# Kernel optimization log

Measured on AMD Instinct MI355X. Metric: run time of the kernel, lower is better.

Reference implementation:

```python
import jax, jax.numpy as jnp
import numpy as np
import math

N = 4264          # all_node_num
B = 256           # batch size
VIS = 784 + 50    # input_node_num + label_node_num
NG = 8            # number of color groups (Pegasus chromatic number is small)
GS = N // NG      # 533 nodes per group
SAMPLE_NUM = 10   # Gibbs sweeps (default 1000 in source; reduced for reference)
AVG_DEG = 15.0    # Pegasus graph degree ~15


def setup_inputs() -> dict:
    key = jax.random.key(0)
    k1, k2, k3, k4 = jax.random.split(key, 4)
    # spin state in {-1, +1}, shape [B, N]
    m = jnp.where(jax.random.normal(k1, (B, N)) >= 0, 1.0, -1.0).astype(jnp.float32)
    # sparse symmetric coupling matrix J: ~AVG_DEG neighbors per node, values randn*0.01
    upper_mask = jnp.triu(jax.random.uniform(k2, (N, N)) < (AVG_DEG / N), k=1)
    Jup = jax.random.normal(k3, (N, N), dtype=jnp.float32) * 0.01 * upper_mask
    J = Jup + Jup.T
    # bias H: log-odds constant on visible nodes, zero on hidden
    h_vis = math.log((VIS / N) / (1.0 - VIS / N))
    H = jnp.zeros((N,), dtype=jnp.float32).at[:VIS].set(h_vis)
    # color groups: disjoint partition of node indices, [NG, GS]
    groups = jax.random.permutation(k4, N).reshape(NG, GS).astype(jnp.int32)
    return {"m": m, "J": J, "H": H, "groups": groups, "sample_num": SAMPLE_NUM}


def reference(m, J, H, groups, sample_num):
    n_groups = groups.shape[0]

    def sweep(m, key):
        keys = jax.random.split(key, n_groups)
        for g in range(n_groups):          # small fixed set of color groups
            idx = groups[g]                # [GS]
            # I = sparse.mm(J[idx], m.T).T + H[idx]  ->  [B, GS]
            I = jnp.einsum('bn,gn->bg', m, J[idx]) + H[idx]
            r = jax.random.uniform(keys[g], I.shape, dtype=I.dtype) * 2.0 - 1.0
            m = m.at[:, idx].set(jnp.sign(jnp.tanh(I) - r))
        return m, None

    iter_keys = jax.random.split(jax.random.key(42), sample_num)
    m, _ = jax.lax.scan(sweep, m, iter_keys)
    return m
```

## Files before the change

### kernel.cpp

```cpp
#include <hip/hip_runtime.h>
#include <hip/hip_bf16.h>
#include <stdint.h>

#define NN 4264
#define BB 256
#define GSZ 533
#define NGRP 8
#define NSWEEP 10
#define NSTEP (NSWEEP * NGRP)
#define DMAX 48
#define DFIX 24
#define NF4 1066
#define NIT 17

struct Keys { unsigned k0[NSTEP]; unsigned k1[NSTEP]; };

#define TF_ROUND(x0, x1, r) { x0 += x1; x1 = (x1 << (r)) | (x1 >> (32 - (r))); x1 ^= x0; }
#define TF_BODY(K0, K1, C0, C1, O0, O1) {                                   \
  unsigned ks0 = (K0), ks1 = (K1), ks2 = (K0) ^ (K1) ^ 0x1BD11BDAu;          \
  unsigned x0 = (C0) + ks0, x1 = (C1) + ks1;                                 \
  TF_ROUND(x0, x1, 13) TF_ROUND(x0, x1, 15) TF_ROUND(x0, x1, 26) TF_ROUND(x0, x1, 6)  \
  x0 += ks1; x1 += ks2 + 1u;                                                 \
  TF_ROUND(x0, x1, 17) TF_ROUND(x0, x1, 29) TF_ROUND(x0, x1, 16) TF_ROUND(x0, x1, 24) \
  x0 += ks2; x1 += ks0 + 2u;                                                 \
  TF_ROUND(x0, x1, 13) TF_ROUND(x0, x1, 15) TF_ROUND(x0, x1, 26) TF_ROUND(x0, x1, 6)  \
  x0 += ks0; x1 += ks1 + 3u;                                                 \
  TF_ROUND(x0, x1, 17) TF_ROUND(x0, x1, 29) TF_ROUND(x0, x1, 16) TF_ROUND(x0, x1, 24) \
  x0 += ks1; x1 += ks2 + 4u;                                                 \
  TF_ROUND(x0, x1, 13) TF_ROUND(x0, x1, 15) TF_ROUND(x0, x1, 26) TF_ROUND(x0, x1, 6)  \
  x0 += ks2; x1 += ks0 + 5u;                                                 \
  (O0) = x0; (O1) = x1; }

static void tf_host(unsigned k0, unsigned k1, unsigned c0, unsigned c1,
                    unsigned* o0, unsigned* o1) {
  unsigned a, b;
  TF_BODY(k0, k1, c0, c1, a, b);
  *o0 = a; *o1 = b;
}

__device__ __forceinline__ void tf_dev(unsigned k0, unsigned k1, unsigned c0, unsigned c1,
                                       unsigned& o0, unsigned& o1) {
  TF_BODY(k0, k1, c0, c1, o0, o1);
}

__global__ __launch_bounds__(256) void build_ell(const float* __restrict__ J,
                                                 const int* __restrict__ groups,
                                                 unsigned* __restrict__ pack4,
                                                 int2* __restrict__ exact8,
                                                 int* __restrict__ deg,
                                                 float* __restrict__ marg) {
  const int wv = threadIdx.x >> 6, lane = threadIdx.x & 63;
  const int p = blockIdx.x * 4 + wv;
  if (p >= NN) return;
  const int node = groups[p];
  const float4* row = (const float4*)(J + (size_t)node * NN);

  float4 vv[NIT];
#pragma unroll
  for (int it = 0; it < NIT; ++it) {
    const int q = it * 64 + lane;
    vv[it] = (q < NF4) ? row[q] : make_float4(0.0f, 0.0f, 0.0f, 0.0f);
  }

  int cnt = 0;
  float asum = 0.0f;
#pragma unroll
  for (int it = 0; it < NIT; ++it) {
    const float4 v = vv[it];
    const int c0 = (it * 64 + lane) * 4;
#define COMP(X, CIDX) {                                                        \
      const bool nz = ((X) != 0.0f);                                           \
      const unsigned long long mk = __ballot(nz);                              \
      const int rk = cnt + __popcll(mk & ((1ull << lane) - 1ull));             \
      if (nz) {                                                                \
        if (rk < DFIX) {                                                       \
          const unsigned bits = __float_as_uint(X);                            \
          const unsigned bf = (bits + 0x7fffu + ((bits >> 16) & 1u)) >> 16;    \
          pack4[(size_t)p * DFIX + rk] = (bf << 16) | ((unsigned)(CIDX) << 2); \
          asum += fabsf(X);                                                    \
        }                                                                      \
        if (rk < DMAX)                                                         \
          exact8[(size_t)p * DMAX + rk] = make_int2((CIDX), __float_as_int(X));\
      }                                                                        \
      cnt += __popcll(mk); }
    COMP(v.x, c0 + 0) COMP(v.y, c0 + 1) COMP(v.z, c0 + 2) COMP(v.w, c0 + 3)
#undef COMP
  }
  for (int k = cnt + lane; k < DFIX; k += 64) pack4[(size_t)p * DFIX + k] = 0u;
  for (int s = 1; s < 64; s <<= 1) asum += __shfl_xor(asum, s, 64);
  if (lane == 0) {
    deg[p] = (cnt > DMAX) ? DMAX : cnt;
    marg[p] = asum * 0.001953125f + 2e-5f;
  }
}

__global__ __launch_bounds__(576) void gibbs(const float* __restrict__ m0,
                                             const float* __restrict__ H,
                                             const int* __restrict__ groups,
                                             const unsigned* __restrict__ pack4,
                                             const int2* __restrict__ exact8,
                                             const int* __restrict__ deg,
                                             const float* __restrict__ marg,
                                             float* __restrict__ out,
                                             Keys keys) {
  __shared__ float m_lds[NN];
  const int b = blockIdx.x;
  const int i = threadIdx.x;
  const bool active = (i < GSZ);

  for (int n = i; n < NN; n += 576) m_lds[n] = m0[(size_t)b * NN + n];

  int nodeg[NGRP];
  float hg[NGRP], mgg[NGRP];
  int dgg[NGRP];
  if (active) {
#pragma unroll
    for (int g = 0; g < NGRP; ++g) {
      const int p = g * GSZ + i;
      nodeg[g] = groups[p];
      hg[g] = H[nodeg[g]];
      dgg[g] = deg[p];
      mgg[g] = marg[p];
    }
  }

  const unsigned c = (unsigned)(b * GSZ + i);

  uint4 w0, w1, w2, w3, w4, w5;
  if (active) {
    const uint4* q = (const uint4*)(pack4 + (size_t)(0 * GSZ + i) * DFIX);
    w0 = q[0]; w1 = q[1]; w2 = q[2]; w3 = q[3]; w4 = q[4]; w5 = q[5];
  }
  __syncthreads();

#pragma unroll 1
  for (int t = 0; t < NSWEEP; ++t) {
#pragma unroll
    for (int g = 0; g < NGRP; ++g) {
      const int step = t * NGRP + g;
      const unsigned k0 = keys.k0[step];
      const unsigned k1 = keys.k1[step];
      float nv = 0.0f;
      uint4 n0, n1, n2, n3, n4, n5;
      if (active) {
        unsigned o0, o1;
        tf_dev(k0, k1, 0u, c, o0, o1);
        const unsigned bits = o0 ^ o1;
        const float u = __uint_as_float((bits >> 9) | 0x3f800000u) - 1.0f;
        const float r = u * 2.0f - 1.0f;

        float a0 = 0.0f, a1 = 0.0f, a2 = 0.0f, a3 = 0.0f;
#define MV(W)  (*(const float*)((const char*)m_lds + ((W) & 0xFFFCu)))
#define ACC(W) \
        a0 += __uint_as_float((W).x & 0xFFFF0000u) * MV((W).x); \
        a1 += __uint_as_float((W).y & 0xFFFF0000u) * MV((W).y); \
        a2 += __uint_as_float((W).z & 0xFFFF0000u) * MV((W).z); \
        a3 += __uint_as_float((W).w & 0xFFFF0000u) * MV((W).w);
        ACC(w0) ACC(w1) ACC(w2) ACC(w3) ACC(w4) ACC(w5)
#undef ACC
#undef MV

        {
          const int gn = (g + 1) & (NGRP - 1);
          const uint4* qn = (const uint4*)(pack4 + (size_t)(gn * GSZ + i) * DFIX);
          n0 = qn[0]; n1 = qn[1]; n2 = qn[2]; n3 = qn[3]; n4 = qn[4]; n5 = qn[5];
        }

        const int dg = dgg[g];
        const int2* ep = exact8 + (size_t)(g * GSZ + i) * DMAX;
        if (__builtin_expect(dg > DFIX, 0)) {
          for (int k = DFIX; k < dg; ++k) {
            const int2 e = ep[k];
            a0 += __int_as_float(e.y) * m_lds[e.x];
          }
        }
        const float I = ((a0 + a1) + (a2 + a3)) + hg[g];

        const float th = tanhf(I);
        const float d = th - r;
        if (__builtin_expect(fabsf(d) > mgg[g], 1)) {
          nv = (d > 0.0f) ? 1.0f : -1.0f;
        } else {
          double I64 = (double)hg[g];
          for (int k = 0; k < dg; ++k) {
            const int2 e = ep[k];
            I64 += (double)__int_as_float(e.y) * (double)m_lds[e.x];
          }
          const double diff = tanh(I64) - (double)r;
          nv = (diff > 0.0) ? 1.0f : ((diff < 0.0) ? -1.0f : 0.0f);
        }
      }
      __syncthreads();
      if (active) m_lds[nodeg[g]] = nv;
      __syncthreads();
      w0 = n0; w1 = n1; w2 = n2; w3 = n3; w4 = n4; w5 = n5;
    }
  }

  for (int n = i; n < NN; n += 576) out[(size_t)b * NN + n] = m_lds[n];
}

extern "C" void kernel_launch(void* const* d_in, const int* in_sizes, int n_in,
                              void* d_out, int out_size, void* d_ws, size_t ws_size,
                              hipStream_t stream) {
  const float* m0     = (const float*)d_in[0];
  const float* J      = (const float*)d_in[1];
  const float* H      = (const float*)d_in[2];
  const int*   groups = (const int*)d_in[3];

  char* ws = (char*)d_ws;
  unsigned* pack4  = (unsigned*)ws;                     ws += (size_t)NN * DFIX * 4;
  int2*     exact8 = (int2*)ws;                         ws += (size_t)NN * DMAX * 8;
  int*      deg    = (int*)ws;                          ws += (size_t)NN * 4;
  float*    marg   = (float*)ws;

  Keys keys;
  for (int t = 0; t < NSWEEP; ++t) {
    unsigned ik0, ik1;
    tf_host(0u, 42u, 0u, (unsigned)t, &ik0, &ik1);
    for (int g = 0; g < NGRP; ++g) {
      unsigned gk0, gk1;
      tf_host(ik0, ik1, 0u, (unsigned)g, &gk0, &gk1);
      keys.k0[t * NGRP + g] = gk0;
      keys.k1[t * NGRP + g] = gk1;
    }
  }

  build_ell<<<(NN + 3) / 4, 256, 0, stream>>>(J, groups, pack4, exact8, deg, marg);
  gibbs<<<BB, 576, 0, stream>>>(m0, H, groups, pack4, exact8, deg, marg,
                                (float*)d_out, keys);
}
```

Baseline: 298.3 us.

## Precompute atanh of random thresholds in a separate kernel, compare in pre-activation space

Adds a kernel that generates every Threefry uniform for all steps and stores atanh(r) in a large workspace table. The Gibbs kernel then compares I against atanh(r), which removes tanhf and the per-step Threefry hash from the sequential loop. It prefetches the next step's value and drops the register double-buffering of the ELL packs, reloading them each step instead. In exchange it pays for an extra launch and for writing and reading about 44 MB of table. It needs enough workspace, otherwise it falls back to the old path.

```diff
diff --git a/kernel.cpp b/kernel.cpp
--- a/kernel.cpp
+++ b/kernel.cpp
@@ -8,6 +8,7 @@
 #define NGRP 8
 #define NSWEEP 10
 #define NSTEP (NSWEEP * NGRP)
+#define NTOT (BB * GSZ)
 #define DMAX 48
 #define DFIX 24
 #define NF4 1066
@@ -41,6 +42,19 @@
 __device__ __forceinline__ void tf_dev(unsigned k0, unsigned k1, unsigned c0, unsigned c1,
                                        unsigned& o0, unsigned& o1) {
   TF_BODY(k0, k1, c0, c1, o0, o1);
+}
+
+__global__ __launch_bounds__(256) void rng_atanh(float* __restrict__ A, Keys keys) {
+  const int step = blockIdx.x / GSZ;
+  const int chunk = blockIdx.x % GSZ;
+  const unsigned c = (unsigned)(chunk * 256 + threadIdx.x);
+  unsigned o0, o1;
+  tf_dev(keys.k0[step], keys.k1[step], 0u, c, o0, o1);
+  const unsigned bits = o0 ^ o1;
+  const float u = __uint_as_float((bits >> 9) | 0x3f800000u) - 1.0f;
+  const float r = u * 2.0f - 1.0f;
+  const float a = 0.5f * logf((1.0f + r) / (1.0f - r));
+  A[(size_t)step * NTOT + c] = a;
 }
 
 __global__ __launch_bounds__(256) void build_ell(const float* __restrict__ J,
@@ -94,6 +108,7 @@
   }
 }
 
+template <bool USE_A>
 __global__ __launch_bounds__(576) void gibbs(const float* __restrict__ m0,
                                              const float* __restrict__ H,
                                              const int* __restrict__ groups,
@@ -101,6 +116,7 @@
                                              const int2* __restrict__ exact8,
                                              const int* __restrict__ deg,
                                              const float* __restrict__ marg,
+                                             const float* __restrict__ Atab,
                                              float* __restrict__ out,
                                              Keys keys) {
   __shared__ float m_lds[NN];
@@ -123,32 +139,29 @@
       mgg[g] = marg[p];
     }
   }
+  __syncthreads();
 
   const unsigned c = (unsigned)(b * GSZ + i);
 
-  uint4 w0, w1, w2, w3, w4, w5;
-  if (active) {
-    const uint4* q = (const uint4*)(pack4 + (size_t)(0 * GSZ + i) * DFIX);
-    w0 = q[0]; w1 = q[1]; w2 = q[2]; w3 = q[3]; w4 = q[4]; w5 = q[5];
-  }
-  __syncthreads();
+  float Acur = 0.0f;
+  if (USE_A && active) Acur = Atab[(size_t)0 * NTOT + c];
 
 #pragma unroll 1
   for (int t = 0; t < NSWEEP; ++t) {
 #pragma unroll
     for (int g = 0; g < NGRP; ++g) {
       const int step = t * NGRP + g;
-      const unsigned k0 = keys.k0[step];
-      const unsigned k1 = keys.k1[step];
       float nv = 0.0f;
-      uint4 n0, n1, n2, n3, n4, n5;
+      float Anext = 0.0f;
       if (active) {
-        unsigned o0, o1;
-        tf_dev(k0, k1, 0u, c, o0, o1);
-        const unsigned bits = o0 ^ o1;
-        const float u = __uint_as_float((bits >> 9) | 0x3f800000u) - 1.0f;
-        const float r = u * 2.0f - 1.0f;
-
+        if (USE_A) {
+          const int sn = (step + 1 < NSTEP) ? step + 1 : step;
+          Anext = Atab[(size_t)sn * NTOT + c];
+        }
+
+        const int p = g * GSZ + i;
+        const uint4* q = (const uint4*)(pack4 + (size_t)p * DFIX);
+        const uint4 w0 = q[0], w1 = q[1], w2 = q[2], w3 = q[3], w4 = q[4], w5 = q[5];
         float a0 = 0.0f, a1 = 0.0f, a2 = 0.0f, a3 = 0.0f;
 #define MV(W)  (*(const float*)((const char*)m_lds + ((W) & 0xFFFCu)))
 #define ACC(W) \
@@ -159,15 +172,8 @@
         ACC(w0) ACC(w1) ACC(w2) ACC(w3) ACC(w4) ACC(w5)
 #undef ACC
 #undef MV
-
-        {
-          const int gn = (g + 1) & (NGRP - 1);
-          const uint4* qn = (const uint4*)(pack4 + (size_t)(gn * GSZ + i) * DFIX);
-          n0 = qn[0]; n1 = qn[1]; n2 = qn[2]; n3 = qn[3]; n4 = qn[4]; n5 = qn[5];
-        }
-
         const int dg = dgg[g];
-        const int2* ep = exact8 + (size_t)(g * GSZ + i) * DMAX;
+        const int2* ep = exact8 + (size_t)p * DMAX;
         if (__builtin_expect(dg > DFIX, 0)) {
           for (int k = DFIX; k < dg; ++k) {
             const int2 e = ep[k];
@@ -176,11 +182,31 @@
         }
         const float I = ((a0 + a1) + (a2 + a3)) + hg[g];
 
-        const float th = tanhf(I);
-        const float d = th - r;
-        if (__builtin_expect(fabsf(d) > mgg[g], 1)) {
+        bool fast;
+        float d;
+        float r = 0.0f;
+        if (USE_A) {
+          d = I - Acur;
+          fast = (fabsf(d) > mgg[g]);
+        } else {
+          unsigned o0, o1;
+          tf_dev(keys.k0[step], keys.k1[step], 0u, c, o0, o1);
+          const unsigned bits = o0 ^ o1;
+          const float u = __uint_as_float((bits >> 9) | 0x3f800000u) - 1.0f;
+          r = u * 2.0f - 1.0f;
+          d = tanhf(I) - r;
+          fast = (fabsf(d) > mgg[g]);
+        }
+        if (__builtin_expect(fast, 1)) {
           nv = (d > 0.0f) ? 1.0f : -1.0f;
         } else {
+          if (USE_A) {
+            unsigned o0, o1;
+            tf_dev(keys.k0[step], keys.k1[step], 0u, c, o0, o1);
+            const unsigned bits = o0 ^ o1;
+            const float u = __uint_as_float((bits >> 9) | 0x3f800000u) - 1.0f;
+            r = u * 2.0f - 1.0f;
+          }
           double I64 = (double)hg[g];
           for (int k = 0; k < dg; ++k) {
             const int2 e = ep[k];
@@ -193,7 +219,7 @@
       __syncthreads();
       if (active) m_lds[nodeg[g]] = nv;
       __syncthreads();
-      w0 = n0; w1 = n1; w2 = n2; w3 = n3; w4 = n4; w5 = n5;
+      Acur = Anext;
     }
   }
 
@@ -212,7 +238,9 @@
   unsigned* pack4  = (unsigned*)ws;                     ws += (size_t)NN * DFIX * 4;
   int2*     exact8 = (int2*)ws;                         ws += (size_t)NN * DMAX * 8;
   int*      deg    = (int*)ws;                          ws += (size_t)NN * 4;
-  float*    marg   = (float*)ws;
+  float*    marg   = (float*)ws;                        ws += (size_t)NN * 4;
+  float*    Atab   = (float*)ws;                        ws += (size_t)NSTEP * NTOT * 4;
+  const bool use_a = ((size_t)(ws - (char*)d_ws) <= ws_size);
 
   Keys keys;
   for (int t = 0; t < NSWEEP; ++t) {
@@ -227,6 +255,12 @@
   }
 
   build_ell<<<(NN + 3) / 4, 256, 0, stream>>>(J, groups, pack4, exact8, deg, marg);
-  gibbs<<<BB, 576, 0, stream>>>(m0, H, groups, pack4, exact8, deg, marg,
-                                (float*)d_out, keys);
-}
+  if (use_a) {
+    rng_atanh<<<NSTEP * GSZ, 256, 0, stream>>>(Atab, keys);
+    gibbs<true><<<BB, 576, 0, stream>>>(m0, H, groups, pack4, exact8, deg, marg,
+                                        Atab, (float*)d_out, keys);
+  } else {
+    gibbs<false><<<BB, 576, 0, stream>>>(m0, H, groups, pack4, exact8, deg, marg,
+                                         Atab, (float*)d_out, keys);
+  }
+}
```

Result: faster. 289.8 us (-2.8%).
